# Performance work log

Hardware: AMD Instinct MI355X
Metric: run time of the kernel (lower is better)

Reference implementation:

```python
import jax, jax.numpy as jnp
import numpy as np

H = 128

def setup_inputs() -> dict:
    key = jax.random.key(0)
    ks = jax.random.split(key, 7)
    x = jax.random.normal(ks[0], (4, 65536, H), dtype=jnp.float32)
    # Linear(3H -> H) and Linear(H -> H), torch-style fan-in init scale
    W1 = jax.random.normal(ks[1], (3 * H, H), dtype=jnp.float32) / np.sqrt(3 * H)
    b1 = jax.random.normal(ks[2], (H,), dtype=jnp.float32) * 0.01
    W2 = jax.random.normal(ks[3], (H, H), dtype=jnp.float32) / np.sqrt(H)
    b2 = jax.random.normal(ks[4], (H,), dtype=jnp.float32) * 0.01
    gamma = jnp.ones((H,), dtype=jnp.float32)
    beta = jnp.zeros((H,), dtype=jnp.float32)
    return {"x": x, "W1": W1, "b1": b1, "W2": W2, "b2": b2, "gamma": gamma, "beta": beta}


def _layernorm(h, gamma, beta, eps=1e-5):
    mu = jnp.mean(h, axis=-1, keepdims=True)
    var = jnp.var(h, axis=-1, keepdims=True)
    return (h - mu) * jax.lax.rsqrt(var + eps) * gamma + beta


def reference(x, W1, b1, W2, b2, gamma, beta):
    # circular neighbor gather along node dim
    prev_x = jnp.roll(x, 1, axis=1)
    next_x = jnp.roll(x, -1, axis=1)
    cat = jnp.concatenate([prev_x, x, next_x], axis=-1)  # [B, N, 3H]
    h = jax.nn.relu(jnp.einsum('bnc,ch->bnh', cat, W1) + b1)
    delta = jnp.einsum('bnh,hk->bnk', h, W2) + b2
    return jax.nn.relu(_layernorm(x + delta, gamma, beta))
```

## Files before the change

kernel.cpp:

```cpp
#include <hip/hip_runtime.h>


typedef __bf16 bf16x8 __attribute__((ext_vector_type(8)));
typedef __bf16 bf16x4 __attribute__((ext_vector_type(4)));
typedef float  f32x4  __attribute__((ext_vector_type(4)));

#define H      128
#define NB     65536
#define TILE   64
#define XS     136
#define HSS    136
#define VS     132
#define NTILES 4096
#define GRID   512

__global__ __launch_bounds__(256, 2)
void cbb_kernel(const float* __restrict__ x, const float* __restrict__ W1,
                const float* __restrict__ b1, const float* __restrict__ W2,
                const float* __restrict__ b2, const float* __restrict__ gamma,
                const float* __restrict__ beta, float* __restrict__ out) {
    __shared__ __align__(16) char raw[(66 * XS + 64 * HSS) * 2];
    __bf16* xs = (__bf16*)raw;
    __bf16* hs = xs + 66 * XS;
    float*  vs = (float*)raw;
    __shared__ __align__(16) __bf16 w2s[16384];
    __shared__ float s_mu[64], s_rs[64], s_gamma[128], s_beta[128];

    const int tid  = threadIdx.x;
    const int wid  = tid >> 6;
    const int lane = tid & 63;
    const int l    = lane & 15;
    const int g    = lane >> 4;
    const int col0 = wid * 32;
    const int c0   = col0 + l;
    const int c1   = col0 + 16 + l;

    if (tid < 128) { s_gamma[tid] = gamma[tid]; s_beta[tid] = beta[tid]; }

    const float b1r0 = b1[c0], b1r1 = b1[c1];
    const float b2r0 = b2[c0], b2r1 = b2[c1];

    bf16x8 w1f[12][2];
#pragma unroll
    for (int ks = 0; ks < 12; ++ks) {
#pragma unroll
        for (int ct = 0; ct < 2; ++ct) {
            const int cc = col0 + ct * 16 + l;
            bf16x8 f;
#pragma unroll
            for (int j = 0; j < 8; ++j)
                f[j] = (__bf16)W1[(ks * 32 + g * 8 + j) * H + cc];
            w1f[ks][ct] = f;
        }
    }

    for (int idx = tid; idx < 16384; idx += 256) {
        const int j  = idx & 7;
        const int ln = (idx >> 3) & 63;
        const int ct = (idx >> 9) & 1;
        const int ks = (idx >> 10) & 3;
        const int w  = idx >> 12;
        const int row = ks * 32 + (ln >> 4) * 8 + j;
        const int col = w * 32 + ct * 16 + (ln & 15);
        w2s[idx] = (__bf16)W2[row * H + col];
    }
    const __bf16* w2w = w2s + wid * 4096;

    float4 xreg[8];
    {
        const int t = blockIdx.x;
        const int b  = t >> 10;
        const int n0 = (t & 1023) << 6;
        const size_t rowbase = (size_t)b * NB;
#pragma unroll
        for (int s = 0; s < 8; ++s) {
            const int q = tid + s * 256;
            const int r = q >> 5, c = q & 31;
            const int grow = (n0 - 1 + r + NB) & (NB - 1);
            xreg[s] = *(const float4*)(x + ((rowbase + grow) * H + c * 4));
        }
    }

    for (int t = blockIdx.x; t < NTILES; t += GRID) {
        const int b  = t >> 10;
        const int n0 = (t & 1023) << 6;
        const size_t rowbase = (size_t)b * NB;

        __syncthreads();

#pragma unroll
        for (int s = 0; s < 8; ++s) {
            const int q = tid + s * 256;
            const int r = q >> 5, c = q & 31;
            bf16x4 v4;
            v4[0] = (__bf16)xreg[s].x; v4[1] = (__bf16)xreg[s].y;
            v4[2] = (__bf16)xreg[s].z; v4[3] = (__bf16)xreg[s].w;
            *(bf16x4*)(xs + r * XS + c * 4) = v4;
        }
        if (tid < 64) {
            const int q = 2048 + tid;
            const int r = q >> 5, c = q & 31;
            const int grow = (n0 - 1 + r + NB) & (NB - 1);
            const float4 f = *(const float4*)(x + ((rowbase + grow) * H + c * 4));
            bf16x4 v4;
            v4[0] = (__bf16)f.x; v4[1] = (__bf16)f.y;
            v4[2] = (__bf16)f.z; v4[3] = (__bf16)f.w;
            *(bf16x4*)(xs + r * XS + c * 4) = v4;
        }
        __syncthreads();

        if (t + GRID < NTILES) {
            const int tn  = t + GRID;
            const int bn  = tn >> 10;
            const int n0n = (tn & 1023) << 6;
            const size_t rbn = (size_t)bn * NB;
#pragma unroll
            for (int s = 0; s < 8; ++s) {
                const int q = tid + s * 256;
                const int r = q >> 5, c = q & 31;
                const int grow = (n0n - 1 + r + NB) & (NB - 1);
                xreg[s] = *(const float4*)(x + ((rbn + grow) * H + c * 4));
            }
        }

        f32x4 acc[4][2];
#pragma unroll
        for (int rt = 0; rt < 4; ++rt)
#pragma unroll
            for (int ct = 0; ct < 2; ++ct)
                acc[rt][ct] = (f32x4){0.f, 0.f, 0.f, 0.f};

#pragma unroll
        for (int rt = 0; rt < 4; ++rt) {
            const int rb = rt * 16 + l;
#pragma unroll
            for (int ks = 0; ks < 12; ++ks) {
                const int k = ks * 32 + g * 8;
                const bf16x8 a = *(const bf16x8*)(xs + (rb + (k >> 7)) * XS + (k & 127));
                acc[rt][0] = __builtin_amdgcn_mfma_f32_16x16x32_bf16(a, w1f[ks][0], acc[rt][0], 0, 0, 0);
                acc[rt][1] = __builtin_amdgcn_mfma_f32_16x16x32_bf16(a, w1f[ks][1], acc[rt][1], 0, 0, 0);
            }
        }

#pragma unroll
        for (int rt = 0; rt < 4; ++rt) {
#pragma unroll
            for (int i = 0; i < 4; ++i) {
                const int row = rt * 16 + g * 4 + i;
                hs[row * HSS + c0] = (__bf16)fmaxf(acc[rt][0][i] + b1r0, 0.f);
                hs[row * HSS + c1] = (__bf16)fmaxf(acc[rt][1][i] + b1r1, 0.f);
            }
        }
        __syncthreads();

        f32x4 acc2[4][2];
#pragma unroll
        for (int rt = 0; rt < 4; ++rt)
#pragma unroll
            for (int ct = 0; ct < 2; ++ct)
                acc2[rt][ct] = (f32x4){0.f, 0.f, 0.f, 0.f};

#pragma unroll
        for (int ks = 0; ks < 4; ++ks) {
            const bf16x8 wf0 = *(const bf16x8*)(w2w + ks * 1024 + lane * 8);
            const bf16x8 wf1 = *(const bf16x8*)(w2w + ks * 1024 + 512 + lane * 8);
#pragma unroll
            for (int rt = 0; rt < 4; ++rt) {
                const bf16x8 a = *(const bf16x8*)(hs + (rt * 16 + l) * HSS + ks * 32 + g * 8);
                acc2[rt][0] = __builtin_amdgcn_mfma_f32_16x16x32_bf16(a, wf0, acc2[rt][0], 0, 0, 0);
                acc2[rt][1] = __builtin_amdgcn_mfma_f32_16x16x32_bf16(a, wf1, acc2[rt][1], 0, 0, 0);
            }
        }

#pragma unroll
        for (int rt = 0; rt < 4; ++rt) {
#pragma unroll
            for (int i = 0; i < 4; ++i) {
                const int row = rt * 16 + g * 4 + i;
                acc2[rt][0][i] += b2r0 + (float)xs[(row + 1) * XS + c0];
                acc2[rt][1][i] += b2r1 + (float)xs[(row + 1) * XS + c1];
            }
        }
        __syncthreads();

#pragma unroll
        for (int rt = 0; rt < 4; ++rt) {
#pragma unroll
            for (int i = 0; i < 4; ++i) {
                const int row = rt * 16 + g * 4 + i;
                vs[row * VS + c0] = acc2[rt][0][i];
                vs[row * VS + c1] = acc2[rt][1][i];
            }
        }
        __syncthreads();

        {
            const int row = tid >> 2;
            const int cb  = (tid & 3) * 32;
            float s = 0.f, qq = 0.f;
#pragma unroll
            for (int c8 = 0; c8 < 8; ++c8) {
                const f32x4 vv = *(const f32x4*)(vs + row * VS + cb + c8 * 4);
#pragma unroll
                for (int e = 0; e < 4; ++e) { s += vv[e]; qq += vv[e] * vv[e]; }
            }
            s  += __shfl_xor(s, 1, 4);  s  += __shfl_xor(s, 2, 4);
            qq += __shfl_xor(qq, 1, 4); qq += __shfl_xor(qq, 2, 4);
            const float muv = s * (1.f / 128.f);
            const float var = qq * (1.f / 128.f) - muv * muv;
            if ((tid & 3) == 0) { s_mu[row] = muv; s_rs[row] = rsqrtf(var + 1e-5f); }
        }
        __syncthreads();

        {
            const int row = tid >> 2;
            const int cb  = (tid & 3) * 32;
            const float muv = s_mu[row], rv = s_rs[row];
            float* op = out + (rowbase + n0 + row) * H + cb;
#pragma unroll
            for (int c8 = 0; c8 < 8; ++c8) {
                const f32x4 vv = *(const f32x4*)(vs + row * VS + cb + c8 * 4);
                const f32x4 gm = *(const f32x4*)(s_gamma + cb + c8 * 4);
                const f32x4 bt = *(const f32x4*)(s_beta + cb + c8 * 4);
                f32x4 o;
#pragma unroll
                for (int e = 0; e < 4; ++e)
                    o[e] = fmaxf((vv[e] - muv) * rv * gm[e] + bt[e], 0.f);
                *(f32x4*)(op + c8 * 4) = o;
            }
        }
    }
}

extern "C" void kernel_launch(void* const* d_in, const int* in_sizes, int n_in,
                              void* d_out, int out_size, void* d_ws, size_t ws_size,
                              hipStream_t stream) {
    const float* x     = (const float*)d_in[0];
    const float* W1    = (const float*)d_in[1];
    const float* b1    = (const float*)d_in[2];
    const float* W2    = (const float*)d_in[3];
    const float* b2    = (const float*)d_in[4];
    const float* gamma = (const float*)d_in[5];
    const float* beta  = (const float*)d_in[6];
    float* out = (float*)d_out;

    cbb_kernel<<<GRID, 256, 0, stream>>>(x, W1, b1, W2, b2, gamma, beta, out);
}
```

Before: 270.3 us.

## Use 8 waves per block with one 16-column strip each, W2 in registers

Doubles the block to 512 threads so each of 8 waves owns a 16-column output strip instead of 32. W2 fragments move from shared memory into registers, which removes the 32KB w2s array. The halo row is now prefetched along with the next tile. This cuts per-thread register and LDS use to allow more resident waves for latency hiding, at the cost of each wave reloading the A fragments from LDS for fewer MFMAs (lower reuse).

```diff
diff --git a/kernel.cpp b/kernel.cpp
--- a/kernel.cpp
+++ b/kernel.cpp
@@ -13,8 +13,9 @@
 #define VS     132
 #define NTILES 4096
 #define GRID   512
-
-__global__ __launch_bounds__(256, 2)
+#define BLK    512
+
+__global__ __launch_bounds__(BLK, 4)
 void cbb_kernel(const float* __restrict__ x, const float* __restrict__ W1,
                 const float* __restrict__ b1, const float* __restrict__ W2,
                 const float* __restrict__ b2, const float* __restrict__ gamma,
@@ -23,7 +24,6 @@
     __bf16* xs = (__bf16*)raw;
     __bf16* hs = xs + 66 * XS;
     float*  vs = (float*)raw;
-    __shared__ __align__(16) __bf16 w2s[16384];
     __shared__ float s_mu[64], s_rs[64], s_gamma[128], s_beta[128];
 
     const int tid  = threadIdx.x;
@@ -31,53 +31,52 @@
     const int lane = tid & 63;
     const int l    = lane & 15;
     const int g    = lane >> 4;
-    const int col0 = wid * 32;
+    const int col0 = wid * 16;
     const int c0   = col0 + l;
-    const int c1   = col0 + 16 + l;
 
     if (tid < 128) { s_gamma[tid] = gamma[tid]; s_beta[tid] = beta[tid]; }
 
-    const float b1r0 = b1[c0], b1r1 = b1[c1];
-    const float b2r0 = b2[c0], b2r1 = b2[c1];
-
-    bf16x8 w1f[12][2];
+    const float b1r0 = b1[c0];
+    const float b2r0 = b2[c0];
+
+    bf16x8 w1f[12];
 #pragma unroll
     for (int ks = 0; ks < 12; ++ks) {
-#pragma unroll
-        for (int ct = 0; ct < 2; ++ct) {
-            const int cc = col0 + ct * 16 + l;
-            bf16x8 f;
-#pragma unroll
-            for (int j = 0; j < 8; ++j)
-                f[j] = (__bf16)W1[(ks * 32 + g * 8 + j) * H + cc];
-            w1f[ks][ct] = f;
-        }
-    }
-
-    for (int idx = tid; idx < 16384; idx += 256) {
-        const int j  = idx & 7;
-        const int ln = (idx >> 3) & 63;
-        const int ct = (idx >> 9) & 1;
-        const int ks = (idx >> 10) & 3;
-        const int w  = idx >> 12;
-        const int row = ks * 32 + (ln >> 4) * 8 + j;
-        const int col = w * 32 + ct * 16 + (ln & 15);
-        w2s[idx] = (__bf16)W2[row * H + col];
-    }
-    const __bf16* w2w = w2s + wid * 4096;
-
-    float4 xreg[8];
+        bf16x8 f;
+#pragma unroll
+        for (int j = 0; j < 8; ++j)
+            f[j] = (__bf16)W1[(ks * 32 + g * 8 + j) * H + c0];
+        w1f[ks] = f;
+    }
+    bf16x8 w2f[4];
+#pragma unroll
+    for (int ks = 0; ks < 4; ++ks) {
+        bf16x8 f;
+#pragma unroll
+        for (int j = 0; j < 8; ++j)
+            f[j] = (__bf16)W2[(ks * 32 + g * 8 + j) * H + c0];
+        w2f[ks] = f;
+    }
+
+    float4 xreg[4];
+    float4 xhalo;
     {
-        const int t = blockIdx.x;
+        const int t  = blockIdx.x;
         const int b  = t >> 10;
         const int n0 = (t & 1023) << 6;
         const size_t rowbase = (size_t)b * NB;
 #pragma unroll
-        for (int s = 0; s < 8; ++s) {
-            const int q = tid + s * 256;
+        for (int s = 0; s < 4; ++s) {
+            const int q = tid + s * BLK;
             const int r = q >> 5, c = q & 31;
             const int grow = (n0 - 1 + r + NB) & (NB - 1);
             xreg[s] = *(const float4*)(x + ((rowbase + grow) * H + c * 4));
+        }
+        if (tid < 64) {
+            const int q = 2048 + tid;
+            const int r = q >> 5, c = q & 31;
+            const int grow = (n0 - 1 + r + NB) & (NB - 1);
+            xhalo = *(const float4*)(x + ((rowbase + grow) * H + c * 4));
         }
     }
 
@@ -89,8 +88,8 @@
         __syncthreads();
 
 #pragma unroll
-        for (int s = 0; s < 8; ++s) {
-            const int q = tid + s * 256;
+        for (int s = 0; s < 4; ++s) {
+            const int q = tid + s * BLK;
             const int r = q >> 5, c = q & 31;
             bf16x4 v4;
             v4[0] = (__bf16)xreg[s].x; v4[1] = (__bf16)xreg[s].y;
@@ -100,11 +99,9 @@
         if (tid < 64) {
             const int q = 2048 + tid;
             const int r = q >> 5, c = q & 31;
-            const int grow = (n0 - 1 + r + NB) & (NB - 1);
-            const float4 f = *(const float4*)(x + ((rowbase + grow) * H + c * 4));
             bf16x4 v4;
-            v4[0] = (__bf16)f.x; v4[1] = (__bf16)f.y;
-            v4[2] = (__bf16)f.z; v4[3] = (__bf16)f.w;
+            v4[0] = (__bf16)xhalo.x; v4[1] = (__bf16)xhalo.y;
+            v4[2] = (__bf16)xhalo.z; v4[3] = (__bf16)xhalo.w;
             *(bf16x4*)(xs + r * XS + c * 4) = v4;
         }
         __syncthreads();
@@ -115,30 +112,32 @@
             const int n0n = (tn & 1023) << 6;
             const size_t rbn = (size_t)bn * NB;
 #pragma unroll
-            for (int s = 0; s < 8; ++s) {
-                const int q = tid + s * 256;
+            for (int s = 0; s < 4; ++s) {
+                const int q = tid + s * BLK;
                 const int r = q >> 5, c = q & 31;
                 const int grow = (n0n - 1 + r + NB) & (NB - 1);
                 xreg[s] = *(const float4*)(x + ((rbn + grow) * H + c * 4));
             }
-        }
-
-        f32x4 acc[4][2];
+            if (tid < 64) {
+                const int q = 2048 + tid;
+                const int r = q >> 5, c = q & 31;
+                const int grow = (n0n - 1 + r + NB) & (NB - 1);
+                xhalo = *(const float4*)(x + ((rbn + grow) * H + c * 4));
+            }
+        }
+
+        f32x4 acc[4];
 #pragma unroll
         for (int rt = 0; rt < 4; ++rt)
-#pragma unroll
-            for (int ct = 0; ct < 2; ++ct)
-                acc[rt][ct] = (f32x4){0.f, 0.f, 0.f, 0.f};
-
-#pragma unroll
-        for (int rt = 0; rt < 4; ++rt) {
-            const int rb = rt * 16 + l;
-#pragma unroll
-            for (int ks = 0; ks < 12; ++ks) {
-                const int k = ks * 32 + g * 8;
-                const bf16x8 a = *(const bf16x8*)(xs + (rb + (k >> 7)) * XS + (k & 127));
-                acc[rt][0] = __builtin_amdgcn_mfma_f32_16x16x32_bf16(a, w1f[ks][0], acc[rt][0], 0, 0, 0);
-                acc[rt][1] = __builtin_amdgcn_mfma_f32_16x16x32_bf16(a, w1f[ks][1], acc[rt][1], 0, 0, 0);
+            acc[rt] = (f32x4){0.f, 0.f, 0.f, 0.f};
+
+#pragma unroll
+        for (int ks = 0; ks < 12; ++ks) {
+            const int k = ks * 32 + g * 8;
+#pragma unroll
+            for (int rt = 0; rt < 4; ++rt) {
+                const bf16x8 a = *(const bf16x8*)(xs + (rt * 16 + l + (k >> 7)) * XS + (k & 127));
+                acc[rt] = __builtin_amdgcn_mfma_f32_16x16x32_bf16(a, w1f[ks], acc[rt], 0, 0, 0);
             }
         }
 
@@ -147,28 +146,22 @@
 #pragma unroll
             for (int i = 0; i < 4; ++i) {
                 const int row = rt * 16 + g * 4 + i;
-                hs[row * HSS + c0] = (__bf16)fmaxf(acc[rt][0][i] + b1r0, 0.f);
-                hs[row * HSS + c1] = (__bf16)fmaxf(acc[rt][1][i] + b1r1, 0.f);
-            }
-        }
-        __syncthreads();
-
-        f32x4 acc2[4][2];
+                hs[row * HSS + c0] = (__bf16)fmaxf(acc[rt][i] + b1r0, 0.f);
+            }
+        }
+        __syncthreads();
+
+        f32x4 acc2[4];
 #pragma unroll
         for (int rt = 0; rt < 4; ++rt)
-#pragma unroll
-            for (int ct = 0; ct < 2; ++ct)
-                acc2[rt][ct] = (f32x4){0.f, 0.f, 0.f, 0.f};
+            acc2[rt] = (f32x4){0.f, 0.f, 0.f, 0.f};
 
 #pragma unroll
         for (int ks = 0; ks < 4; ++ks) {
-            const bf16x8 wf0 = *(const bf16x8*)(w2w + ks * 1024 + lane * 8);
-            const bf16x8 wf1 = *(const bf16x8*)(w2w + ks * 1024 + 512 + lane * 8);
 #pragma unroll
             for (int rt = 0; rt < 4; ++rt) {
                 const bf16x8 a = *(const bf16x8*)(hs + (rt * 16 + l) * HSS + ks * 32 + g * 8);
-                acc2[rt][0] = __builtin_amdgcn_mfma_f32_16x16x32_bf16(a, wf0, acc2[rt][0], 0, 0, 0);
-                acc2[rt][1] = __builtin_amdgcn_mfma_f32_16x16x32_bf16(a, wf1, acc2[rt][1], 0, 0, 0);
+                acc2[rt] = __builtin_amdgcn_mfma_f32_16x16x32_bf16(a, w2f[ks], acc2[rt], 0, 0, 0);
             }
         }
 
@@ -177,8 +170,7 @@
 #pragma unroll
             for (int i = 0; i < 4; ++i) {
                 const int row = rt * 16 + g * 4 + i;
-                acc2[rt][0][i] += b2r0 + (float)xs[(row + 1) * XS + c0];
-                acc2[rt][1][i] += b2r1 + (float)xs[(row + 1) * XS + c1];
+                acc2[rt][i] += b2r0 + (float)xs[(row + 1) * XS + c0];
             }
         }
         __syncthreads();
@@ -188,37 +180,36 @@
 #pragma unroll
             for (int i = 0; i < 4; ++i) {
                 const int row = rt * 16 + g * 4 + i;
-                vs[row * VS + c0] = acc2[rt][0][i];
-                vs[row * VS + c1] = acc2[rt][1][i];
+                vs[row * VS + c0] = acc2[rt][i];
             }
         }
         __syncthreads();
 
         {
-            const int row = tid >> 2;
-            const int cb  = (tid & 3) * 32;
+            const int row = tid >> 3;
+            const int cb  = (tid & 7) * 16;
             float s = 0.f, qq = 0.f;
 #pragma unroll
-            for (int c8 = 0; c8 < 8; ++c8) {
+            for (int c8 = 0; c8 < 4; ++c8) {
                 const f32x4 vv = *(const f32x4*)(vs + row * VS + cb + c8 * 4);
 #pragma unroll
                 for (int e = 0; e < 4; ++e) { s += vv[e]; qq += vv[e] * vv[e]; }
             }
-            s  += __shfl_xor(s, 1, 4);  s  += __shfl_xor(s, 2, 4);
-            qq += __shfl_xor(qq, 1, 4); qq += __shfl_xor(qq, 2, 4);
+            s  += __shfl_xor(s, 1, 8);  s  += __shfl_xor(s, 2, 8);  s  += __shfl_xor(s, 4, 8);
+            qq += __shfl_xor(qq, 1, 8); qq += __shfl_xor(qq, 2, 8); qq += __shfl_xor(qq, 4, 8);
             const float muv = s * (1.f / 128.f);
             const float var = qq * (1.f / 128.f) - muv * muv;
-            if ((tid & 3) == 0) { s_mu[row] = muv; s_rs[row] = rsqrtf(var + 1e-5f); }
+            if ((tid & 7) == 0) { s_mu[row] = muv; s_rs[row] = rsqrtf(var + 1e-5f); }
         }
         __syncthreads();
 
         {
-            const int row = tid >> 2;
-            const int cb  = (tid & 3) * 32;
+            const int row = tid >> 3;
+            const int cb  = (tid & 7) * 16;
             const float muv = s_mu[row], rv = s_rs[row];
             float* op = out + (rowbase + n0 + row) * H + cb;
 #pragma unroll
-            for (int c8 = 0; c8 < 8; ++c8) {
+            for (int c8 = 0; c8 < 4; ++c8) {
                 const f32x4 vv = *(const f32x4*)(vs + row * VS + cb + c8 * 4);
                 const f32x4 gm = *(const f32x4*)(s_gamma + cb + c8 * 4);
                 const f32x4 bt = *(const f32x4*)(s_beta + cb + c8 * 4);
@@ -244,5 +235,5 @@
     const float* beta  = (const float*)d_in[6];
     float* out = (float*)d_out;
 
-    cbb_kernel<<<GRID, 256, 0, stream>>>(x, W1, b1, W2, b2, gamma, beta, out);
+    cbb_kernel<<<GRID, BLK, 0, stream>>>(x, W1, b1, W2, b2, gamma, beta, out);
 }
```

After: 354.9 us. 1.31x slower.

## Prefetch halo rows, reorder MFMA loop, raise priority, fuse LayerNorm passes

Applied to the files above, without the earlier changes.

The two halo rows of each tile are now loaded into a register alongside the main prefetch, instead of being fetched synchronously inside the loop. The first GEMM loop is reordered to iterate k outermost, and both MFMA loops are wrapped in s_setprio to favour the matrix-issuing waves. The LayerNorm statistics and output passes are merged: row values are kept in registers, one barrier and the shared mu/rstd arrays are dropped, and columns are interleaved across the four threads of a row. The vs row stride changes from 132 to 133 floats to reduce bank conflicts. An odd stride leaves the 16-byte vector LDS reads misaligned on odd rows, which could split those accesses or be unsafe.

```diff
diff --git a/kernel.cpp b/kernel.cpp
--- a/kernel.cpp
+++ b/kernel.cpp
@@ -10,7 +10,7 @@
 #define TILE   64
 #define XS     136
 #define HSS    136
-#define VS     132
+#define VS     133
 #define NTILES 4096
 #define GRID   512
 
@@ -24,7 +24,7 @@
     __bf16* hs = xs + 66 * XS;
     float*  vs = (float*)raw;
     __shared__ __align__(16) __bf16 w2s[16384];
-    __shared__ float s_mu[64], s_rs[64], s_gamma[128], s_beta[128];
+    __shared__ float s_gamma[128], s_beta[128];
 
     const int tid  = threadIdx.x;
     const int wid  = tid >> 6;
@@ -67,8 +67,9 @@
     const __bf16* w2w = w2s + wid * 4096;
 
     float4 xreg[8];
+    float4 xhalo;
     {
-        const int t = blockIdx.x;
+        const int t  = blockIdx.x;
         const int b  = t >> 10;
         const int n0 = (t & 1023) << 6;
         const size_t rowbase = (size_t)b * NB;
@@ -78,6 +79,12 @@
             const int r = q >> 5, c = q & 31;
             const int grow = (n0 - 1 + r + NB) & (NB - 1);
             xreg[s] = *(const float4*)(x + ((rowbase + grow) * H + c * 4));
+        }
+        if (tid < 64) {
+            const int q = 2048 + tid;
+            const int r = q >> 5, c = q & 31;
+            const int grow = (n0 - 1 + r + NB) & (NB - 1);
+            xhalo = *(const float4*)(x + ((rowbase + grow) * H + c * 4));
         }
     }
 
@@ -100,11 +107,9 @@
         if (tid < 64) {
             const int q = 2048 + tid;
             const int r = q >> 5, c = q & 31;
-            const int grow = (n0 - 1 + r + NB) & (NB - 1);
-            const float4 f = *(const float4*)(x + ((rowbase + grow) * H + c * 4));
             bf16x4 v4;
-            v4[0] = (__bf16)f.x; v4[1] = (__bf16)f.y;
-            v4[2] = (__bf16)f.z; v4[3] = (__bf16)f.w;
+            v4[0] = (__bf16)xhalo.x; v4[1] = (__bf16)xhalo.y;
+            v4[2] = (__bf16)xhalo.z; v4[3] = (__bf16)xhalo.w;
             *(bf16x4*)(xs + r * XS + c * 4) = v4;
         }
         __syncthreads();
@@ -121,6 +126,12 @@
                 const int grow = (n0n - 1 + r + NB) & (NB - 1);
                 xreg[s] = *(const float4*)(x + ((rbn + grow) * H + c * 4));
             }
+            if (tid < 64) {
+                const int q = 2048 + tid;
+                const int r = q >> 5, c = q & 31;
+                const int grow = (n0n - 1 + r + NB) & (NB - 1);
+                xhalo = *(const float4*)(x + ((rbn + grow) * H + c * 4));
+            }
         }
 
         f32x4 acc[4][2];
@@ -130,17 +141,19 @@
             for (int ct = 0; ct < 2; ++ct)
                 acc[rt][ct] = (f32x4){0.f, 0.f, 0.f, 0.f};
 
-#pragma unroll
-        for (int rt = 0; rt < 4; ++rt) {
-            const int rb = rt * 16 + l;
-#pragma unroll
-            for (int ks = 0; ks < 12; ++ks) {
-                const int k = ks * 32 + g * 8;
-                const bf16x8 a = *(const bf16x8*)(xs + (rb + (k >> 7)) * XS + (k & 127));
+        __builtin_amdgcn_s_setprio(1);
+#pragma unroll
+        for (int ks = 0; ks < 12; ++ks) {
+            const int k  = ks * 32 + g * 8;
+            const int ro = k >> 7, kc = k & 127;
+#pragma unroll
+            for (int rt = 0; rt < 4; ++rt) {
+                const bf16x8 a = *(const bf16x8*)(xs + (rt * 16 + l + ro) * XS + kc);
                 acc[rt][0] = __builtin_amdgcn_mfma_f32_16x16x32_bf16(a, w1f[ks][0], acc[rt][0], 0, 0, 0);
                 acc[rt][1] = __builtin_amdgcn_mfma_f32_16x16x32_bf16(a, w1f[ks][1], acc[rt][1], 0, 0, 0);
             }
         }
+        __builtin_amdgcn_s_setprio(0);
 
 #pragma unroll
         for (int rt = 0; rt < 4; ++rt) {
@@ -160,6 +173,7 @@
             for (int ct = 0; ct < 2; ++ct)
                 acc2[rt][ct] = (f32x4){0.f, 0.f, 0.f, 0.f};
 
+        __builtin_amdgcn_s_setprio(1);
 #pragma unroll
         for (int ks = 0; ks < 4; ++ks) {
             const bf16x8 wf0 = *(const bf16x8*)(w2w + ks * 1024 + lane * 8);
@@ -171,6 +185,7 @@
                 acc2[rt][1] = __builtin_amdgcn_mfma_f32_16x16x32_bf16(a, wf1, acc2[rt][1], 0, 0, 0);
             }
         }
+        __builtin_amdgcn_s_setprio(0);
 
 #pragma unroll
         for (int rt = 0; rt < 4; ++rt) {
@@ -196,37 +211,30 @@
 
         {
             const int row = tid >> 2;
-            const int cb  = (tid & 3) * 32;
+            const int q4  = (tid & 3) * 4;
+            f32x4 vv[8];
             float s = 0.f, qq = 0.f;
 #pragma unroll
             for (int c8 = 0; c8 < 8; ++c8) {
-                const f32x4 vv = *(const f32x4*)(vs + row * VS + cb + c8 * 4);
-#pragma unroll
-                for (int e = 0; e < 4; ++e) { s += vv[e]; qq += vv[e] * vv[e]; }
+                vv[c8] = *(const f32x4*)(vs + row * VS + c8 * 16 + q4);
+#pragma unroll
+                for (int e = 0; e < 4; ++e) { s += vv[c8][e]; qq += vv[c8][e] * vv[c8][e]; }
             }
             s  += __shfl_xor(s, 1, 4);  s  += __shfl_xor(s, 2, 4);
             qq += __shfl_xor(qq, 1, 4); qq += __shfl_xor(qq, 2, 4);
             const float muv = s * (1.f / 128.f);
             const float var = qq * (1.f / 128.f) - muv * muv;
-            if ((tid & 3) == 0) { s_mu[row] = muv; s_rs[row] = rsqrtf(var + 1e-5f); }
-        }
-        __syncthreads();
-
-        {
-            const int row = tid >> 2;
-            const int cb  = (tid & 3) * 32;
-            const float muv = s_mu[row], rv = s_rs[row];
-            float* op = out + (rowbase + n0 + row) * H + cb;
+            const float rv  = rsqrtf(var + 1e-5f);
+            float* op = out + (rowbase + n0 + row) * H;
 #pragma unroll
             for (int c8 = 0; c8 < 8; ++c8) {
-                const f32x4 vv = *(const f32x4*)(vs + row * VS + cb + c8 * 4);
-                const f32x4 gm = *(const f32x4*)(s_gamma + cb + c8 * 4);
-                const f32x4 bt = *(const f32x4*)(s_beta + cb + c8 * 4);
+                const f32x4 gm = *(const f32x4*)(s_gamma + c8 * 16 + q4);
+                const f32x4 bt = *(const f32x4*)(s_beta  + c8 * 16 + q4);
                 f32x4 o;
 #pragma unroll
                 for (int e = 0; e < 4; ++e)
-                    o[e] = fmaxf((vv[e] - muv) * rv * gm[e] + bt[e], 0.f);
-                *(f32x4*)(op + c8 * 4) = o;
+                    o[e] = fmaxf((vv[c8][e] - muv) * rv * gm[e] + bt[e], 0.f);
+                *(f32x4*)(op + c8 * 16 + q4) = o;
             }
         }
     }
```

Measured after the change: 264.6 us. 2.1% less time.
